# Optimization experiments

Measured on AMD Instinct MI355X. Metric: run time of the kernel, lower is better.

## Reference

```python
import jax, jax.numpy as jnp
import numpy as np

F = 1024      # features
CF = 768      # context_features
H = 8         # num_heads
D = 64        # head_features
MID = H * D   # 512
SCALE = D ** -0.5


def _ln(x, g, b):
    m = jnp.mean(x, axis=-1, keepdims=True)
    v = jnp.var(x, axis=-1, keepdims=True)
    return (x - m) / jnp.sqrt(v + 1e-5) * g + b


def _attention(x, ctx, ng, nb, ncg, ncb, wq, wkv, wo, bo):
    # pre-norms (Attention.forward)
    xn = _ln(x, ng, nb)
    cn = _ln(ctx, ncg, ncb)
    q = xn @ wq                              # [b, n, MID]
    k, v = jnp.split(cn @ wkv, 2, axis=-1)   # [b, m, MID] each
    b, n, _ = q.shape
    m = k.shape[1]
    q = q.reshape(b, n, H, D).transpose(0, 2, 1, 3)  # b h n d
    k = k.reshape(b, m, H, D).transpose(0, 2, 1, 3)
    v = v.reshape(b, m, H, D).transpose(0, 2, 1, 3)
    sim = jnp.einsum('bhnd,bhmd->bhnm', q, k) * SCALE   # use_rel_pos=False
    attn = jax.nn.softmax(sim, axis=-1)
    out = jnp.einsum('bhnm,bhmd->bhnd', attn, v)
    out = out.transpose(0, 2, 1, 3).reshape(b, n, MID)
    return out @ wo + bo


def setup_inputs() -> dict:
    key = jax.random.key(0)
    ks = jax.random.split(key, 16)
    s = 0.02
    inp = {
        'x': jax.random.normal(ks[0], (4, 2048, F), jnp.float32),
        'context': jax.random.normal(ks[1], (4, 512, CF), jnp.float32),
        # self-attention params
        'sa_ng': jnp.ones((F,), jnp.float32),
        'sa_nb': jnp.zeros((F,), jnp.float32),
        'sa_ncg': jnp.ones((F,), jnp.float32),
        'sa_ncb': jnp.zeros((F,), jnp.float32),
        'sa_wq': jax.random.normal(ks[2], (F, MID), jnp.float32) * s,
        'sa_wkv': jax.random.normal(ks[3], (F, 2 * MID), jnp.float32) * s,
        'sa_wo': jax.random.normal(ks[4], (MID, F), jnp.float32) * s,
        'sa_bo': jnp.zeros((F,), jnp.float32),
        # cross-attention params
        'ca_ng': jnp.ones((F,), jnp.float32),
        'ca_nb': jnp.zeros((F,), jnp.float32),
        'ca_ncg': jnp.ones((CF,), jnp.float32),
        'ca_ncb': jnp.zeros((CF,), jnp.float32),
        'ca_wq': jax.random.normal(ks[5], (F, MID), jnp.float32) * s,
        'ca_wkv': jax.random.normal(ks[6], (CF, 2 * MID), jnp.float32) * s,
        'ca_wo': jax.random.normal(ks[7], (MID, F), jnp.float32) * s,
        'ca_bo': jnp.zeros((F,), jnp.float32),
    }
    return inp


def reference(x, context,
              sa_ng, sa_nb, sa_ncg, sa_ncb, sa_wq, sa_wkv, sa_wo, sa_bo,
              ca_ng, ca_nb, ca_ncg, ca_ncb, ca_wq, ca_wkv, ca_wo, ca_bo):
    # AttentionBlock.forward: x = self_attn(x) + x; x = cross_attn(x, ctx) + x
    x = _attention(x, x, sa_ng, sa_nb, sa_ncg, sa_ncb, sa_wq, sa_wkv, sa_wo, sa_bo) + x
    x = _attention(x, context, ca_ng, ca_nb, ca_ncg, ca_ncb, ca_wq, ca_wkv, ca_wo, ca_bo) + x
    return x
```

## Files before the change

kernel.cpp:

```cpp
#include <hip/hip_runtime.h>
#include <hip/hip_bf16.h>

typedef __bf16 bf16x8 __attribute__((ext_vector_type(8)));
typedef float  f32x4  __attribute__((ext_vector_type(4)));
typedef float  f32x16 __attribute__((ext_vector_type(16)));

#define MFMA16(a, b, c) __builtin_amdgcn_mfma_f32_16x16x32_bf16((a), (b), (c), 0, 0, 0)
#define MFMA32(a, b, c) __builtin_amdgcn_mfma_f32_32x32x16_bf16((a), (b), (c), 0, 0, 0)

__device__ __forceinline__ float fast_exp2(float x) {
#if __has_builtin(__builtin_amdgcn_exp2f)
    return __builtin_amdgcn_exp2f(x);
#else
    return exp2f(x);
#endif
}

__device__ __forceinline__ void async16(void* lds, const void* g) {
    __builtin_amdgcn_global_load_lds(
        (const __attribute__((address_space(1))) unsigned int*)g,
        (__attribute__((address_space(3))) unsigned int*)lds, 16, 0, 0);
}

__device__ __forceinline__ void tconv_tile(const float* __restrict__ W,
                                           __bf16* __restrict__ WT,
                                           int K, int N, int id, int nbx,
                                           __bf16 (*t)[65]) {
    int n0 = (id % nbx) * 64, k0 = (id / nbx) * 64;
    int tx = threadIdx.x & 63, ty = threadIdx.x >> 6;
#pragma unroll
    for (int r = ty; r < 64; r += 4)
        t[r][tx] = (__bf16)W[(size_t)(k0 + r) * N + n0 + tx];
    __syncthreads();
#pragma unroll
    for (int rr = ty; rr < 64; rr += 4)
        WT[(size_t)(n0 + rr) * K + k0 + tx] = t[tx][rr];
}

__global__ __launch_bounds__(256) void tconv6_kernel(
    const float* W0, __bf16* T0, const float* W1, __bf16* T1,
    const float* W2, __bf16* T2, const float* W3, __bf16* T3,
    const float* W4, __bf16* T4, const float* W5, __bf16* T5) {
    __shared__ __bf16 t[64][65];
    int id = blockIdx.x;
    if (id < 128)      tconv_tile(W0, T0, 1024, 512,  id,       8,  t);
    else if (id < 384) tconv_tile(W1, T1, 1024, 1024, id - 128, 16, t);
    else if (id < 512) tconv_tile(W2, T2, 512,  1024, id - 384, 16, t);
    else if (id < 640) tconv_tile(W3, T3, 1024, 512,  id - 512, 8,  t);
    else if (id < 832) tconv_tile(W4, T4, 768,  1024, id - 640, 16, t);
    else               tconv_tile(W5, T5, 512,  1024, id - 832, 16, t);
}

template <int C>
__device__ __forceinline__ void ln_body(const float* __restrict__ xr,
                                        const float* __restrict__ g,
                                        const float* __restrict__ b,
                                        __bf16* __restrict__ orow,
                                        float* p1, float* p2) {
    constexpr int NP = (C == 1024) ? 4 : 3;
    float v[NP], s1 = 0.f, s2 = 0.f;
    if constexpr (C == 1024) {
        float4 f = *(const float4*)&xr[threadIdx.x * 4];
        v[0] = f.x; v[1] = f.y; v[2] = f.z; v[3] = f.w;
#pragma unroll
        for (int i = 0; i < 4; i++) { s1 += v[i]; s2 += v[i] * v[i]; }
    } else {
#pragma unroll
        for (int i = 0; i < 3; i++) {
            v[i] = xr[threadIdx.x + i * 256];
            s1 += v[i]; s2 += v[i] * v[i];
        }
    }
#pragma unroll
    for (int off = 1; off < 64; off <<= 1) {
        s1 += __shfl_xor(s1, off);
        s2 += __shfl_xor(s2, off);
    }
    int wave = threadIdx.x >> 6;
    if ((threadIdx.x & 63) == 0) { p1[wave] = s1; p2[wave] = s2; }
    __syncthreads();
    s1 = p1[0] + p1[1] + p1[2] + p1[3];
    s2 = p2[0] + p2[1] + p2[2] + p2[3];
    float mean = s1 / C;
    float rstd = rsqrtf(s2 / C - mean * mean + 1e-5f);
    if constexpr (C == 1024) {
        union { __bf16 h[4]; unsigned long long u; } pk;
#pragma unroll
        for (int i = 0; i < 4; i++) {
            int c = threadIdx.x * 4 + i;
            pk.h[i] = (__bf16)((v[i] - mean) * rstd * g[c] + b[c]);
        }
        *(unsigned long long*)&orow[threadIdx.x * 4] = pk.u;
    } else {
#pragma unroll
        for (int i = 0; i < 3; i++) {
            int c = threadIdx.x + i * 256;
            orow[c] = (__bf16)((v[i] - mean) * rstd * g[c] + b[c]);
        }
    }
}

__global__ __launch_bounds__(256) void ln2_kernel(const float* __restrict__ x,
                                                  const float* __restrict__ g1,
                                                  const float* __restrict__ b1,
                                                  const float* __restrict__ g2,
                                                  const float* __restrict__ b2,
                                                  __bf16* __restrict__ o1,
                                                  __bf16* __restrict__ o2) {
    constexpr int C = 1024;
    int row = blockIdx.x;
    const float* xr = x + (size_t)row * C;
    float4 f = *(const float4*)&xr[threadIdx.x * 4];
    float v[4] = {f.x, f.y, f.z, f.w};
    float s1 = 0.f, s2 = 0.f;
#pragma unroll
    for (int i = 0; i < 4; i++) { s1 += v[i]; s2 += v[i] * v[i]; }
#pragma unroll
    for (int off = 1; off < 64; off <<= 1) {
        s1 += __shfl_xor(s1, off);
        s2 += __shfl_xor(s2, off);
    }
    __shared__ float p1[4], p2[4];
    int wave = threadIdx.x >> 6;
    if ((threadIdx.x & 63) == 0) { p1[wave] = s1; p2[wave] = s2; }
    __syncthreads();
    s1 = p1[0] + p1[1] + p1[2] + p1[3];
    s2 = p2[0] + p2[1] + p2[2] + p2[3];
    float mean = s1 / C;
    float rstd = rsqrtf(s2 / C - mean * mean + 1e-5f);
    union { __bf16 h[4]; unsigned long long u; } pk1, pk2;
#pragma unroll
    for (int i = 0; i < 4; i++) {
        int c = threadIdx.x * 4 + i;
        float nv = (v[i] - mean) * rstd;
        pk1.h[i] = (__bf16)(nv * g1[c] + b1[c]);
        pk2.h[i] = (__bf16)(nv * g2[c] + b2[c]);
    }
    *(unsigned long long*)&o1[(size_t)row * C + threadIdx.x * 4] = pk1.u;
    *(unsigned long long*)&o2[(size_t)row * C + threadIdx.x * 4] = pk2.u;
}

__global__ __launch_bounds__(256) void ln_cross_kernel(
    const float* __restrict__ x1, const float* __restrict__ g1, const float* __restrict__ b1,
    __bf16* __restrict__ o1,
    const float* __restrict__ ctx, const float* __restrict__ g2, const float* __restrict__ b2,
    __bf16* __restrict__ o2, int rows1) {
    __shared__ float p1[4], p2[4];
    int id = blockIdx.x;
    if (id < rows1) {
        ln_body<1024>(x1 + (size_t)id * 1024, g1, b1, o1 + (size_t)id * 1024, p1, p2);
    } else {
        int row = id - rows1;
        ln_body<768>(ctx + (size_t)row * 768, g2, b2, o2 + (size_t)row * 768, p1, p2);
    }
}

template <int EPI>
__device__ __forceinline__ void gemm_core(const __bf16* __restrict__ A,
                                          const __bf16* __restrict__ BT,
                                          void* __restrict__ Cout,
                                          int N, int K, int bm, int bn,
                                          const float* __restrict__ bias,
                                          const float* __restrict__ res,
                                          float scale,
                                          __bf16* Al, __bf16* Bl) {
    int tid = threadIdx.x;
    int lane = tid & 63, wave = tid >> 6;
    int quad = lane >> 4, l15 = lane & 15;
    int wm = wave >> 1, wn = wave & 1;
    const __bf16* Ab = A + (size_t)(bm * 128) * K;
    const __bf16* Bb = BT + (size_t)(bn * 128) * K;
    f32x4 acc[4][4] = {};
    for (int k0 = 0; k0 < K; k0 += 64) {
#pragma unroll
        for (int j = 0; j < 4; j++) {
            int sbase = wave * 256 + j * 64;
            int s = sbase + lane;
            int r = s >> 3, c = (s & 7) ^ (r & 7);
            async16((char*)Al + sbase * 16, &Ab[(size_t)r * K + k0 + c * 8]);
            async16((char*)Bl + sbase * 16, &Bb[(size_t)r * K + k0 + c * 8]);
        }
        __syncthreads();
#pragma unroll
        for (int ks = 0; ks < 2; ks++) {
            bf16x8 a[4], b[4];
#pragma unroll
            for (int i = 0; i < 4; i++) {
                int row = wm * 64 + i * 16 + l15;
                a[i] = *(const bf16x8*)&Al[row * 64 + ((ks * 4 + quad) ^ (row & 7)) * 8];
            }
#pragma unroll
            for (int t = 0; t < 4; t++) {
                int row = wn * 64 + t * 16 + l15;
                b[t] = *(const bf16x8*)&Bl[row * 64 + ((ks * 4 + quad) ^ (row & 7)) * 8];
            }
#pragma unroll
            for (int i = 0; i < 4; i++)
#pragma unroll
                for (int t = 0; t < 4; t++) acc[i][t] = MFMA16(a[i], b[t], acc[i][t]);
        }
        __syncthreads();
    }
#pragma unroll
    for (int i = 0; i < 4; i++) {
#pragma unroll
        for (int t = 0; t < 4; t++) {
#pragma unroll
            for (int r = 0; r < 4; r++) {
                int row = bm * 128 + wm * 64 + i * 16 + quad * 4 + r;
                int col = bn * 128 + wn * 64 + t * 16 + l15;
                float vv = acc[i][t][r];
                if (EPI == 0) {
                    ((__bf16*)Cout)[(size_t)row * N + col] = (__bf16)(vv * scale);
                } else {
                    ((float*)Cout)[(size_t)row * N + col] =
                        vv + bias[col] + res[(size_t)row * N + col];
                }
            }
        }
    }
}

template <int EPI>
__global__ __launch_bounds__(256) void gemm_bt(const __bf16* __restrict__ A,
                                               const __bf16* __restrict__ BT,
                                               void* __restrict__ Cout,
                                               int M, int N, int K,
                                               const float* __restrict__ bias,
                                               const float* __restrict__ res) {
    __shared__ __align__(16) __bf16 Al[128 * 64];
    __shared__ __align__(16) __bf16 Bl[128 * 64];
    gemm_core<EPI>(A, BT, Cout, N, K, blockIdx.x, blockIdx.y, bias, res, 1.0f, Al, Bl);
}

__global__ __launch_bounds__(256) void gemm_fused3(
    const __bf16* A0, const __bf16* B0, __bf16* C0, int N0, int K0, int nbn0, float sc0,
    const __bf16* A1, const __bf16* B1, __bf16* C1, int N1, int K1, int nbn1, float sc1,
    const __bf16* A2, const __bf16* B2, __bf16* C2, int N2, int K2, int nbn2, float sc2,
    int c0, int c1) {
    __shared__ __align__(16) __bf16 Al[128 * 64];
    __shared__ __align__(16) __bf16 Bl[128 * 64];
    int id = blockIdx.x;
    if (id < c0) {
        gemm_core<0>(A0, B0, C0, N0, K0, id / nbn0, id % nbn0, nullptr, nullptr, sc0, Al, Bl);
    } else if (id < c1) {
        id -= c0;
        gemm_core<0>(A1, B1, C1, N1, K1, id / nbn1, id % nbn1, nullptr, nullptr, sc1, Al, Bl);
    } else {
        id -= c1;
        gemm_core<0>(A2, B2, C2, N2, K2, id / nbn2, id % nbn2, nullptr, nullptr, sc2, Al, Bl);
    }
}

__global__ __launch_bounds__(128) void flash_kernel(const __bf16* __restrict__ q,
                                                    const __bf16* __restrict__ kb,
                                                    const __bf16* __restrict__ vt,
                                                    __bf16* __restrict__ out,
                                                    int n, int m) {
    __shared__ __align__(16) __bf16 Qs[128 * 64];
    __shared__ __align__(16) __bf16 Ks[64 * 64];
    __shared__ __align__(16) __bf16 VTs[64 * 64];
    int tid = threadIdx.x;
    int lane = tid & 63, w = tid >> 6;
    int l31 = lane & 31, l5 = lane >> 5;
    int qt = blockIdx.x, h = blockIdx.y, b = blockIdx.z;
    const size_t BM = (size_t)gridDim.z * m;

#pragma unroll
    for (int j = 0; j < 8; j++) {
        int sbase = w * 512 + j * 64;
        int s = sbase + lane;
        int r = s >> 3, c = (s & 7) ^ (r & 7);
        async16((char*)Qs + sbase * 16,
                &q[(size_t)(b * n + qt * 128 + r) * 512 + h * 64 + c * 8]);
    }

    f32x16 acc[2][2] = {};
    float l_acc[2] = {0.f, 0.f};

    int nkt = m / 64;
    for (int kt = 0; kt < nkt; kt++) {
#pragma unroll
        for (int j = 0; j < 4; j++) {
            int sbase = w * 256 + j * 64;
            int s = sbase + lane;
            int r = s >> 3, c = (s & 7) ^ (r & 7);
            async16((char*)Ks + sbase * 16,
                    &kb[(size_t)(b * m + kt * 64 + r) * 512 + h * 64 + c * 8]);
            async16((char*)VTs + sbase * 16,
                    &vt[(size_t)(h * 64 + r) * BM + b * m + kt * 64 + c * 8]);
        }
        __syncthreads();

#pragma unroll
        for (int mt = 0; mt < 2; mt++) {
            f32x16 sacc[2] = {};
#pragma unroll
            for (int c = 0; c < 4; c++) {
                int krow = mt * 32 + l31;
                bf16x8 ak = *(const bf16x8*)&Ks[krow * 64 + ((2 * c + l5) ^ (krow & 7)) * 8];
#pragma unroll
                for (int nt = 0; nt < 2; nt++) {
                    int qrow = w * 64 + nt * 32 + l31;
                    bf16x8 bq = *(const bf16x8*)&Qs[qrow * 64 + ((2 * c + l5) ^ (qrow & 7)) * 8];
                    sacc[nt] = MFMA32(ak, bq, sacc[nt]);
                }
            }
            unsigned long long pk[2][4], sh[2][4];
#pragma unroll
            for (int nt = 0; nt < 2; nt++) {
#pragma unroll
                for (int s = 0; s < 4; s++) {
                    float e0 = fast_exp2(sacc[nt][s * 4 + 0]);
                    float e1 = fast_exp2(sacc[nt][s * 4 + 1]);
                    float e2 = fast_exp2(sacc[nt][s * 4 + 2]);
                    float e3 = fast_exp2(sacc[nt][s * 4 + 3]);
                    l_acc[nt] += (e0 + e1) + (e2 + e3);
                    union { __bf16 hh[4]; unsigned long long u; } u;
                    u.hh[0] = (__bf16)e0; u.hh[1] = (__bf16)e1;
                    u.hh[2] = (__bf16)e2; u.hh[3] = (__bf16)e3;
                    pk[nt][s] = u.u;
                }
#pragma unroll
                for (int s = 0; s < 4; s++)
                    sh[nt][s] = __shfl_xor((unsigned long long)pk[nt][s], 32);
            }
#pragma unroll
            for (int c2 = 0; c2 < 2; c2++) {
#pragma unroll
                for (int nt = 0; nt < 2; nt++) {
                    int s0 = 2 * c2, s1 = 2 * c2 + 1;
                    unsigned long long h0 = (l5 == 0) ? pk[nt][s0] : sh[nt][s1];
                    unsigned long long h1 = (l5 == 0) ? sh[nt][s0] : pk[nt][s1];
                    union { unsigned long long u[2]; bf16x8 v; } bu;
                    bu.u[0] = h0; bu.u[1] = h1;
#pragma unroll
                    for (int mtd = 0; mtd < 2; mtd++) {
                        int drow = mtd * 32 + l31;
                        int kchunk = 2 * (2 * mt + c2) + l5;
                        bf16x8 av = *(const bf16x8*)&VTs[drow * 64 + (kchunk ^ (drow & 7)) * 8];
                        acc[mtd][nt] = MFMA32(av, bu.v, acc[mtd][nt]);
                    }
                }
            }
        }
        __syncthreads();
    }

    float linv[2];
#pragma unroll
    for (int nt = 0; nt < 2; nt++) {
        float tot = l_acc[nt] + __shfl_xor(l_acc[nt], 32);
        linv[nt] = 1.0f / tot;
    }
#pragma unroll
    for (int nt = 0; nt < 2; nt++) {
        size_t qrow = (size_t)(b * n + qt * 128 + w * 64 + nt * 32 + l31);
#pragma unroll
        for (int mtd = 0; mtd < 2; mtd++) {
#pragma unroll
            for (int s = 0; s < 4; s++) {
                union { __bf16 hh[4]; unsigned long long u; } u;
#pragma unroll
                for (int r = 0; r < 4; r++)
                    u.hh[r] = (__bf16)(acc[mtd][nt][s * 4 + r] * linv[nt]);
                int d = mtd * 32 + s * 8 + l5 * 4;
                *(unsigned long long*)&out[qrow * 512 + h * 64 + d] = u.u;
            }
        }
    }
}

extern "C" void kernel_launch(void* const* d_in, const int* in_sizes, int n_in,
                              void* d_out, int out_size, void* d_ws, size_t ws_size,
                              hipStream_t stream) {
    const float* x      = (const float*)d_in[0];
    const float* ctx    = (const float*)d_in[1];
    const float* sa_ng  = (const float*)d_in[2];
    const float* sa_nb  = (const float*)d_in[3];
    const float* sa_ncg = (const float*)d_in[4];
    const float* sa_ncb = (const float*)d_in[5];
    const float* sa_wq  = (const float*)d_in[6];
    const float* sa_wkv = (const float*)d_in[7];
    const float* sa_wo  = (const float*)d_in[8];
    const float* sa_bo  = (const float*)d_in[9];
    const float* ca_ng  = (const float*)d_in[10];
    const float* ca_nb  = (const float*)d_in[11];
    const float* ca_ncg = (const float*)d_in[12];
    const float* ca_ncb = (const float*)d_in[13];
    const float* ca_wq  = (const float*)d_in[14];
    const float* ca_wkv = (const float*)d_in[15];
    const float* ca_wo  = (const float*)d_in[16];
    const float* ca_bo  = (const float*)d_in[17];
    float* out = (float*)d_out;

    const int B = 4, N = 2048, M = 512, F = 1024, CF = 768, MID = 512;
    const int ROWS = B * N;
    const int CROWS = B * M;
    const float QSCALE = 0.125f * 1.4426950408889634f;

    char* ws = (char*)d_ws;
    size_t off = 0;
    auto alloc = [&](size_t bytes) {
        void* p = ws + off;
        off = (off + bytes + 255) & ~(size_t)255;
        return p;
    };
    __bf16* wqT   = (__bf16*)alloc((size_t)MID * F * 2);
    __bf16* wkvT  = (__bf16*)alloc((size_t)(2 * MID) * F * 2);
    __bf16* woT   = (__bf16*)alloc((size_t)F * MID * 2);
    __bf16* cwqT  = (__bf16*)alloc((size_t)MID * F * 2);
    __bf16* cwkvT = (__bf16*)alloc((size_t)(2 * MID) * CF * 2);
    __bf16* cwoT  = (__bf16*)alloc((size_t)F * MID * 2);
    __bf16* xn1   = (__bf16*)alloc((size_t)ROWS * F * 2);
    __bf16* xn2   = (__bf16*)alloc((size_t)ROWS * F * 2);
    __bf16* qb    = (__bf16*)alloc((size_t)ROWS * MID * 2);
    __bf16* kb    = (__bf16*)alloc((size_t)ROWS * MID * 2);
    __bf16* vt    = (__bf16*)alloc((size_t)MID * ROWS * 2);
    __bf16* ao    = (__bf16*)alloc((size_t)ROWS * MID * 2);
    float*  x1    = (float*)alloc((size_t)ROWS * F * 4);
    (void)ws_size; (void)in_sizes; (void)n_in; (void)out_size;

    dim3 blk(256);
    dim3 fblk(128);

    tconv6_kernel<<<dim3(960), blk, 0, stream>>>(
        sa_wq, wqT, sa_wkv, wkvT, sa_wo, woT, ca_wq, cwqT, ca_wkv, cwkvT, ca_wo, cwoT);

    ln2_kernel<<<dim3(ROWS), blk, 0, stream>>>(x, sa_ng, sa_nb, sa_ncg, sa_ncb, xn1, xn2);
    {
        int c0 = (ROWS / 128) * (MID / 128);
        int c1 = c0 + (ROWS / 128) * (MID / 128);
        int c2 = c1 + (MID / 128) * (ROWS / 128);
        gemm_fused3<<<dim3(c2), blk, 0, stream>>>(
            xn1, wqT, qb, MID, F, MID / 128, QSCALE,
            xn2, wkvT, kb, MID, F, MID / 128, 1.0f,
            wkvT + (size_t)MID * F, xn2, vt, ROWS, F, ROWS / 128, 1.0f,
            c0, c1);
    }
    flash_kernel<<<dim3(N / 128, 8, B), fblk, 0, stream>>>(qb, kb, vt, ao, N, N);
    gemm_bt<1><<<dim3(ROWS / 128, F / 128), blk, 0, stream>>>(
        ao, woT, x1, ROWS, F, MID, sa_bo, x);

    ln_cross_kernel<<<dim3(ROWS + CROWS), blk, 0, stream>>>(
        x1, ca_ng, ca_nb, xn1, ctx, ca_ncg, ca_ncb, xn2, ROWS);
    {
        int c0 = (ROWS / 128) * (MID / 128);
        int c1 = c0 + (CROWS / 128) * (MID / 128);
        int c2 = c1 + (MID / 128) * (CROWS / 128);
        gemm_fused3<<<dim3(c2), blk, 0, stream>>>(
            xn1, cwqT, qb, MID, F, MID / 128, QSCALE,
            xn2, cwkvT, kb, MID, CF, MID / 128, 1.0f,
            cwkvT + (size_t)MID * CF, xn2, vt, CROWS, CF, CROWS / 128, 1.0f,
            c0, c1);
    }
    flash_kernel<<<dim3(N / 128, 8, B), fblk, 0, stream>>>(qb, kb, vt, ao, N, M);
    gemm_bt<1><<<dim3(ROWS / 128, F / 128), blk, 0, stream>>>(
        ao, cwoT, out, ROWS, F, MID, ca_bo, x1);
}
```

Baseline: 327.0 us.

## Split flash attention query tile across four waves instead of two

The flash kernel now runs with 256 threads, so each of four waves owns 32 query rows instead of 64, with accumulators reduced to match. Q fragments are hoisted into registers once per key tile, and the Q/K/V async load loops are redistributed over the four waves. This is meant to raise per-CU parallelism and latency hiding while cutting register pressure per wave. In exchange, each key/V tile loaded into LDS is reused by fewer MFMAs per wave, and more waves contend at each barrier.

```diff
diff --git a/kernel.cpp b/kernel.cpp
--- a/kernel.cpp
+++ b/kernel.cpp
@@ -252,7 +252,7 @@
     }
 }
 
-__global__ __launch_bounds__(128) void flash_kernel(const __bf16* __restrict__ q,
+__global__ __launch_bounds__(256) void flash_kernel(const __bf16* __restrict__ q,
                                                     const __bf16* __restrict__ kb,
                                                     const __bf16* __restrict__ vt,
                                                     __bf16* __restrict__ out,
@@ -265,24 +265,25 @@
     int l31 = lane & 31, l5 = lane >> 5;
     int qt = blockIdx.x, h = blockIdx.y, b = blockIdx.z;
     const size_t BM = (size_t)gridDim.z * m;
-
-#pragma unroll
-    for (int j = 0; j < 8; j++) {
-        int sbase = w * 512 + j * 64;
+    const int qrow = w * 32 + l31;
+
+#pragma unroll
+    for (int j = 0; j < 4; j++) {
+        int sbase = j * 256 + w * 64;
         int s = sbase + lane;
         int r = s >> 3, c = (s & 7) ^ (r & 7);
         async16((char*)Qs + sbase * 16,
                 &q[(size_t)(b * n + qt * 128 + r) * 512 + h * 64 + c * 8]);
     }
 
-    f32x16 acc[2][2] = {};
-    float l_acc[2] = {0.f, 0.f};
+    f32x16 acc[2] = {};
+    float l_acc = 0.f;
 
     int nkt = m / 64;
     for (int kt = 0; kt < nkt; kt++) {
 #pragma unroll
-        for (int j = 0; j < 4; j++) {
-            int sbase = w * 256 + j * 64;
+        for (int j = 0; j < 2; j++) {
+            int sbase = j * 256 + w * 64;
             int s = sbase + lane;
             int r = s >> 3, c = (s & 7) ^ (r & 7);
             async16((char*)Ks + sbase * 16,
@@ -292,81 +293,75 @@
         }
         __syncthreads();
 
+        bf16x8 bq[4];
+#pragma unroll
+        for (int c = 0; c < 4; c++)
+            bq[c] = *(const bf16x8*)&Qs[qrow * 64 + ((2 * c + l5) ^ (qrow & 7)) * 8];
+        f32x16 sacc[2] = {};
 #pragma unroll
         for (int mt = 0; mt < 2; mt++) {
-            f32x16 sacc[2] = {};
+            int krow = mt * 32 + l31;
 #pragma unroll
             for (int c = 0; c < 4; c++) {
-                int krow = mt * 32 + l31;
                 bf16x8 ak = *(const bf16x8*)&Ks[krow * 64 + ((2 * c + l5) ^ (krow & 7)) * 8];
-#pragma unroll
-                for (int nt = 0; nt < 2; nt++) {
-                    int qrow = w * 64 + nt * 32 + l31;
-                    bf16x8 bq = *(const bf16x8*)&Qs[qrow * 64 + ((2 * c + l5) ^ (qrow & 7)) * 8];
-                    sacc[nt] = MFMA32(ak, bq, sacc[nt]);
+                sacc[mt] = MFMA32(ak, bq[c], sacc[mt]);
+            }
+        }
+
+        unsigned long long pk[2][4], sh[2][4];
+#pragma unroll
+        for (int mt = 0; mt < 2; mt++) {
+#pragma unroll
+            for (int s = 0; s < 4; s++) {
+                float e0 = fast_exp2(sacc[mt][s * 4 + 0]);
+                float e1 = fast_exp2(sacc[mt][s * 4 + 1]);
+                float e2 = fast_exp2(sacc[mt][s * 4 + 2]);
+                float e3 = fast_exp2(sacc[mt][s * 4 + 3]);
+                l_acc += (e0 + e1) + (e2 + e3);
+                union { __bf16 hh[4]; unsigned long long u; } u;
+                u.hh[0] = (__bf16)e0; u.hh[1] = (__bf16)e1;
+                u.hh[2] = (__bf16)e2; u.hh[3] = (__bf16)e3;
+                pk[mt][s] = u.u;
+            }
+#pragma unroll
+            for (int s = 0; s < 4; s++)
+                sh[mt][s] = __shfl_xor((unsigned long long)pk[mt][s], 32);
+        }
+
+#pragma unroll
+        for (int mt = 0; mt < 2; mt++) {
+#pragma unroll
+            for (int c2 = 0; c2 < 2; c2++) {
+                int s0 = 2 * c2, s1 = 2 * c2 + 1;
+                unsigned long long h0 = (l5 == 0) ? pk[mt][s0] : sh[mt][s1];
+                unsigned long long h1 = (l5 == 0) ? sh[mt][s0] : pk[mt][s1];
+                union { unsigned long long u[2]; bf16x8 v; } bu;
+                bu.u[0] = h0; bu.u[1] = h1;
+                int kchunk = 2 * (2 * mt + c2) + l5;
+#pragma unroll
+                for (int mtd = 0; mtd < 2; mtd++) {
+                    int drow = mtd * 32 + l31;
+                    bf16x8 av = *(const bf16x8*)&VTs[drow * 64 + (kchunk ^ (drow & 7)) * 8];
+                    acc[mtd] = MFMA32(av, bu.v, acc[mtd]);
                 }
             }
-            unsigned long long pk[2][4], sh[2][4];
-#pragma unroll
-            for (int nt = 0; nt < 2; nt++) {
-#pragma unroll
-                for (int s = 0; s < 4; s++) {
-                    float e0 = fast_exp2(sacc[nt][s * 4 + 0]);
-                    float e1 = fast_exp2(sacc[nt][s * 4 + 1]);
-                    float e2 = fast_exp2(sacc[nt][s * 4 + 2]);
-                    float e3 = fast_exp2(sacc[nt][s * 4 + 3]);
-                    l_acc[nt] += (e0 + e1) + (e2 + e3);
-                    union { __bf16 hh[4]; unsigned long long u; } u;
-                    u.hh[0] = (__bf16)e0; u.hh[1] = (__bf16)e1;
-                    u.hh[2] = (__bf16)e2; u.hh[3] = (__bf16)e3;
-                    pk[nt][s] = u.u;
-                }
-#pragma unroll
-                for (int s = 0; s < 4; s++)
-                    sh[nt][s] = __shfl_xor((unsigned long long)pk[nt][s], 32);
-            }
-#pragma unroll
-            for (int c2 = 0; c2 < 2; c2++) {
-#pragma unroll
-                for (int nt = 0; nt < 2; nt++) {
-                    int s0 = 2 * c2, s1 = 2 * c2 + 1;
-                    unsigned long long h0 = (l5 == 0) ? pk[nt][s0] : sh[nt][s1];
-                    unsigned long long h1 = (l5 == 0) ? sh[nt][s0] : pk[nt][s1];
-                    union { unsigned long long u[2]; bf16x8 v; } bu;
-                    bu.u[0] = h0; bu.u[1] = h1;
-#pragma unroll
-                    for (int mtd = 0; mtd < 2; mtd++) {
-                        int drow = mtd * 32 + l31;
-                        int kchunk = 2 * (2 * mt + c2) + l5;
-                        bf16x8 av = *(const bf16x8*)&VTs[drow * 64 + (kchunk ^ (drow & 7)) * 8];
-                        acc[mtd][nt] = MFMA32(av, bu.v, acc[mtd][nt]);
-                    }
-                }
-            }
         }
         __syncthreads();
     }
 
-    float linv[2];
-#pragma unroll
-    for (int nt = 0; nt < 2; nt++) {
-        float tot = l_acc[nt] + __shfl_xor(l_acc[nt], 32);
-        linv[nt] = 1.0f / tot;
-    }
-#pragma unroll
-    for (int nt = 0; nt < 2; nt++) {
-        size_t qrow = (size_t)(b * n + qt * 128 + w * 64 + nt * 32 + l31);
-#pragma unroll
-        for (int mtd = 0; mtd < 2; mtd++) {
-#pragma unroll
-            for (int s = 0; s < 4; s++) {
-                union { __bf16 hh[4]; unsigned long long u; } u;
-#pragma unroll
-                for (int r = 0; r < 4; r++)
-                    u.hh[r] = (__bf16)(acc[mtd][nt][s * 4 + r] * linv[nt]);
-                int d = mtd * 32 + s * 8 + l5 * 4;
-                *(unsigned long long*)&out[qrow * 512 + h * 64 + d] = u.u;
-            }
+    float tot = l_acc + __shfl_xor(l_acc, 32);
+    float linv = 1.0f / tot;
+    size_t qg = (size_t)(b * n + qt * 128 + w * 32 + l31);
+#pragma unroll
+    for (int mtd = 0; mtd < 2; mtd++) {
+#pragma unroll
+        for (int s = 0; s < 4; s++) {
+            union { __bf16 hh[4]; unsigned long long u; } u;
+#pragma unroll
+            for (int r = 0; r < 4; r++)
+                u.hh[r] = (__bf16)(acc[mtd][s * 4 + r] * linv);
+            int d = mtd * 32 + s * 8 + l5 * 4;
+            *(unsigned long long*)&out[qg * 512 + h * 64 + d] = u.u;
         }
     }
 }
@@ -422,7 +417,6 @@
     (void)ws_size; (void)in_sizes; (void)n_in; (void)out_size;
 
     dim3 blk(256);
-    dim3 fblk(128);
 
     tconv6_kernel<<<dim3(960), blk, 0, stream>>>(
         sa_wq, wqT, sa_wkv, wkvT, sa_wo, woT, ca_wq, cwqT, ca_wkv, cwkvT, ca_wo, cwoT);
@@ -438,7 +432,7 @@
             wkvT + (size_t)MID * F, xn2, vt, ROWS, F, ROWS / 128, 1.0f,
             c0, c1);
     }
-    flash_kernel<<<dim3(N / 128, 8, B), fblk, 0, stream>>>(qb, kb, vt, ao, N, N);
+    flash_kernel<<<dim3(N / 128, 8, B), blk, 0, stream>>>(qb, kb, vt, ao, N, N);
     gemm_bt<1><<<dim3(ROWS / 128, F / 128), blk, 0, stream>>>(
         ao, woT, x1, ROWS, F, MID, sa_bo, x);
 
@@ -454,7 +448,7 @@
             cwkvT + (size_t)MID * CF, xn2, vt, CROWS, CF, CROWS / 128, 1.0f,
             c0, c1);
     }
-    flash_kernel<<<dim3(N / 128, 8, B), fblk, 0, stream>>>(qb, kb, vt, ao, N, M);
+    flash_kernel<<<dim3(N / 128, 8, B), blk, 0, stream>>>(qb, kb, vt, ao, N, M);
     gemm_bt<1><<<dim3(ROWS / 128, F / 128), blk, 0, stream>>>(
         ao, cwoT, out, ROWS, F, MID, ca_bo, x1);
 }
```

After: 324.3 us. No clear change (-0.8%).
